# Optimization experiments

Hardware: AMD Instinct MI355X
Metric: run time of the kernel (lower is better)

The kernel has to match this reference:

```python
import math
import jax, jax.numpy as jnp
import numpy as np

TOPK = 2
CAPACITY_FACTOR = 1.25
MIN_CAPACITY = 4


def setup_inputs() -> dict:
    key = jax.random.key(0)
    k1, k2, k3, k4, k5 = jax.random.split(key, 5)
    B, T, H, W, D = 2, 8, 16, 16, 2048
    E, I = 16, 2048
    s = 1.0 / math.sqrt(D)
    return {
        "hidden_states": jax.random.normal(k1, (B, T, H, W, D), dtype=jnp.float32),
        "wg_weight": jax.random.normal(k2, (E, D), dtype=jnp.float32) * s,
        "gate_proj": jax.random.normal(k3, (E, I, D), dtype=jnp.float32) * s,
        "up_proj": jax.random.normal(k4, (E, I, D), dtype=jnp.float32) * s,
        "down_proj": jax.random.normal(k5, (E, D, I), dtype=jnp.float32) * (1.0 / math.sqrt(I)),
    }


def _moe_forward(x, wg, gp, up, dp):
    B, T, H, W, D = x.shape
    S = T * H * W
    # core_shape=(1,1,1): indexing tokens == calculate tokens, flatten (T,H,W)
    tokens = x.reshape(B, S, D).transpose(1, 0, 2).reshape(-1, D)  # (N, D)
    N = tokens.shape[0]
    E = wg.shape[0]

    logits = tokens.astype(jnp.float32) @ wg.T              # (N, E)
    gates = jax.nn.softmax(logits, axis=1)                  # (N, E)

    # static expert capacity: topk * max(ceil(N/E * cf), min_capacity)
    cap = TOPK * max(math.ceil(N / E * CAPACITY_FACTOR), MIN_CAPACITY)

    _, expert_index = jax.lax.top_k(gates, TOPK)            # (N, k)
    expert_mask = jax.nn.one_hot(expert_index, E, dtype=jnp.int32)  # (N, k, E)

    # aux load-balance loss (computed for fidelity)
    mask_aux = expert_mask.max(axis=1).astype(jnp.float32)  # (N, E)
    l_aux = (E ** 2) * jnp.mean(jnp.mean(mask_aux, axis=0) * jnp.mean(gates, axis=0))

    # normalize top-k probabilities (norm_topk_prob=True, topk>1)
    gates_s = jnp.clip(jnp.einsum('nke,ne->n', expert_mask.astype(gates.dtype), gates),
                       jnp.finfo(gates.dtype).eps)
    router_probs = gates / gates_s[:, None]                 # (N, E)

    # token priority: cumsum over (topk*N) flattened in topk-major order
    em = expert_mask.transpose(1, 0, 2).reshape(TOPK * N, E)  # (kN, E)
    tp = jnp.cumsum(em, axis=0) * em - 1
    tp = tp.reshape(TOPK, N, E).transpose(1, 0, 2).max(axis=1)  # (N, E)
    valid = (tp >= 0) & (tp < cap)
    tp = jnp.where(valid, tp, 0)
    dispatch_mask = (tp[:, :, None] == jnp.arange(cap)[None, None, :]) & valid[:, :, None]  # (N,E,C) bool
    combine_weights = router_probs[:, :, None] * dispatch_mask  # (N, E, C)

    # dispatch -> expert FFN (SwiGLU) -> combine
    dm = dispatch_mask.astype(tokens.dtype)
    dispatched = jnp.einsum('nec,nd->ecd', dm, tokens)      # (E, C, D)
    gate_out = jax.nn.silu(jnp.einsum('ecd,eid->eci', dispatched, gp))
    up_out = jnp.einsum('ecd,eid->eci', dispatched, up)
    expert_out = jnp.einsum('eci,edi->ecd', gate_out * up_out, dp)  # (E, C, D)
    combined = jnp.einsum('nec,ecd->nd', combine_weights, expert_out)  # (N, D)

    y = combined.reshape(S, B, D).transpose(1, 0, 2).reshape(B, T, H, W, D)
    return y, l_aux


def reference(hidden_states, wg_weight, gate_proj, up_proj, down_proj):
    y, _l_aux = _moe_forward(hidden_states, wg_weight, gate_proj, up_proj, down_proj)
    return y
```

## Files before the change

kernel.cpp:

```cpp
#include <hip/hip_runtime.h>
#include <hip/hip_bf16.h>
#include <cstdint>
#include <cstddef>

#define NTOK 4096
#define NEXP 16
#define DIM  2048
#define IDIM 2048
#define CAP  640
#define SEQ  2048

typedef float v4f __attribute__((ext_vector_type(4)));
typedef short v8s __attribute__((ext_vector_type(8)));

__device__ __forceinline__ unsigned short f2b(float x) {
    union { float f; unsigned u; } c; c.f = x;
    unsigned r = c.u + 0x7FFFu + ((c.u >> 16) & 1u);
    return (unsigned short)(r >> 16);
}
__device__ __forceinline__ float b2f(unsigned short x) {
    union { unsigned u; float f; } c; c.u = ((unsigned)x) << 16;
    return c.f;
}

__device__ __forceinline__ void async16(const void* g, void* l) {
    __builtin_amdgcn_global_load_lds(
        (const __attribute__((address_space(1))) unsigned int*)g,
        (__attribute__((address_space(3))) unsigned int*)l,
        16, 0, 0);
}

__global__ __launch_bounds__(256) void router_kernel(
    const float* __restrict__ hidden, const float* __restrict__ wg,
    int* __restrict__ top1, int* __restrict__ top2,
    float* __restrict__ w1, float* __restrict__ w2)
{
    int wid  = threadIdx.x >> 6;
    int lane = threadIdx.x & 63;
    int n = blockIdx.x * 4 + wid;
    int e = lane & 15;
    int chunk = lane >> 4;
    const float* tok  = hidden + ((size_t)(n & 1) * SEQ + (n >> 1)) * DIM;
    const float* wrow = wg + (size_t)e * DIM;
    float acc = 0.f;
    int d0 = chunk * (DIM / 4);
    #pragma unroll 4
    for (int d = d0; d < d0 + DIM / 4; d += 4) {
        float4 t4 = *(const float4*)(tok + d);
        float4 g4 = *(const float4*)(wrow + d);
        acc += t4.x * g4.x + t4.y * g4.y + t4.z * g4.z + t4.w * g4.w;
    }
    acc += __shfl_down(acc, 32);
    acc += __shfl_down(acc, 16);
    float v = acc;
    float v1 = v; int i1 = e;
    #pragma unroll
    for (int off = 8; off; off >>= 1) {
        float ov = __shfl_xor(v1, off);
        int   oi = __shfl_xor(i1, off);
        if (ov > v1 || (ov == v1 && oi < i1)) { v1 = ov; i1 = oi; }
    }
    float v2 = (e == i1) ? -INFINITY : v; int i2 = e;
    #pragma unroll
    for (int off = 8; off; off >>= 1) {
        float ov = __shfl_xor(v2, off);
        int   oi = __shfl_xor(i2, off);
        if (ov > v2 || (ov == v2 && oi < i2)) { v2 = ov; i2 = oi; }
    }
    if (lane == 0) {
        float e2v = expf(v2 - v1);
        float inv = 1.f / (1.f + e2v);
        top1[n] = i1; top2[n] = i2;
        w1[n] = inv;  w2[n] = e2v * inv;
    }
}

__global__ __launch_bounds__(1024) void slot_kernel(
    const int* __restrict__ top1, const int* __restrict__ top2,
    int* __restrict__ slot1, int* __restrict__ slot2,
    int* __restrict__ exp_tok, int* __restrict__ counts)
{
    int w = threadIdx.x >> 6;
    int lane = threadIdx.x & 63;
    unsigned long long below = (lane == 0) ? 0ull : ((~0ull) >> (64 - lane));
    int base = 0;
    for (int c = 0; c < NTOK / 64; ++c) {
        int n = c * 64 + lane;
        bool p = (top1[n] == w);
        unsigned long long m = __ballot(p);
        if (p) {
            int s = base + __popcll(m & below);
            slot1[n] = s;
            if (s < CAP) exp_tok[w * CAP + s] = n;
        }
        base += __popcll(m);
    }
    for (int c = 0; c < NTOK / 64; ++c) {
        int n = c * 64 + lane;
        bool p = (top2[n] == w);
        unsigned long long m = __ballot(p);
        if (p) {
            int s = base + __popcll(m & below);
            slot2[n] = s;
            if (s < CAP) exp_tok[w * CAP + s] = n;
        }
        base += __popcll(m);
    }
    if (lane == 0) counts[w] = base < CAP ? base : CAP;
}

__global__ __launch_bounds__(256) void dispatch_kernel(
    const float* __restrict__ hidden, const int* __restrict__ exp_tok,
    const int* __restrict__ counts, unsigned short* __restrict__ disp)
{
    int s = blockIdx.x, e = blockIdx.y;
    unsigned short* dst = disp + ((size_t)e * CAP + s) * DIM + threadIdx.x * 8;
    if (s < counts[e]) {
        int n = exp_tok[e * CAP + s];
        const float* src = hidden + ((size_t)(n & 1) * SEQ + (n >> 1)) * DIM + threadIdx.x * 8;
        float4 a = *(const float4*)src;
        float4 b = *(const float4*)(src + 4);
        v8s o;
        o[0] = (short)f2b(a.x); o[1] = (short)f2b(a.y);
        o[2] = (short)f2b(a.z); o[3] = (short)f2b(a.w);
        o[4] = (short)f2b(b.x); o[5] = (short)f2b(b.y);
        o[6] = (short)f2b(b.z); o[7] = (short)f2b(b.w);
        *(v8s*)dst = o;
    } else {
        v8s z = {0, 0, 0, 0, 0, 0, 0, 0};
        *(v8s*)dst = z;
    }
}

#define BK 64

template<int NW, int ROUNDS>
__device__ __forceinline__ void stage_a(
    const unsigned short* __restrict__ gbase, int grow0, int k0, int rs,
    unsigned short* lds, int wv, int ln)
{
    int sr = ln >> 3;
    int cb = ln & 7;
    #pragma unroll
    for (int p = 0; p < ROUNDS; ++p) {
        int r = p * (NW * 8) + wv * 8 + sr;
        const unsigned short* g = gbase + (size_t)(grow0 + r) * rs + k0 + ((cb ^ (r & 7)) << 3);
        async16(g, lds + (p * (NW * 8) + wv * 8) * 64);
    }
}

template<int NT, int ROUNDS>
__device__ __forceinline__ void issue_bx(
    const float* __restrict__ gbase, int grow0, int k0, int rs,
    float4* regs, int tid)
{
    int cb = tid & 7;
    int r0 = tid >> 3;
    #pragma unroll
    for (int p = 0; p < ROUNDS; ++p) {
        const float* g = gbase + (size_t)(grow0 + p * (NT / 8) + r0) * rs + k0 + (cb << 3);
        regs[2 * p]     = *(const float4*)g;
        regs[2 * p + 1] = *(const float4*)(g + 4);
    }
}

template<int NT, int ROUNDS>
__device__ __forceinline__ void write_bx(
    const float4* regs, unsigned short* lds, int tid)
{
    int cb = tid & 7;
    int r0 = tid >> 3;
    #pragma unroll
    for (int p = 0; p < ROUNDS; ++p) {
        int r = p * (NT / 8) + r0;
        float4 x = regs[2 * p], y = regs[2 * p + 1];
        v8s o;
        o[0] = (short)f2b(x.x); o[1] = (short)f2b(x.y);
        o[2] = (short)f2b(x.z); o[3] = (short)f2b(x.w);
        o[4] = (short)f2b(y.x); o[5] = (short)f2b(y.y);
        o[6] = (short)f2b(y.z); o[7] = (short)f2b(y.w);
        *(v8s*)&lds[r * 64 + ((cb ^ (r & 7)) << 3)] = o;
    }
}

__device__ __forceinline__ void grid_decomp3(int bid, int& mi, int& ni, int& e) {
    int swz = (bid & 7) * 96 + (bid >> 3);
    mi = swz % 3;
    int t = swz / 3;
    ni = t & 15;
    e  = t >> 4;
}

__global__ __launch_bounds__(512, 2) void gateup_kernel(
    const unsigned short* __restrict__ disp, const float* __restrict__ gp,
    const float* __restrict__ up, const int* __restrict__ counts,
    unsigned short* __restrict__ hbuf)
{
    extern __shared__ unsigned short smem[];
    unsigned short* As0 = smem;
    unsigned short* As1 = smem + 16384;
    unsigned short* Bgs = smem + 32768;
    unsigned short* Bus = smem + 40960;
    int mi, ni, e;
    grid_decomp3(blockIdx.x, mi, ni, e);
    int m0 = mi * 256;
    if (m0 >= counts[e]) return;
    int n0 = ni * 128;
    int tid = threadIdx.x;
    int wv = tid >> 6, ln = tid & 63;
    int wm = wv >> 1, wn = wv & 1;
    int lrow = ln & 15, quad = ln >> 4;
    int sw = lrow & 7;

    const unsigned short* Ab = disp + (size_t)e * CAP * DIM;
    const float* Gb = gp + (size_t)e * IDIM * DIM;
    const float* Ub = up + (size_t)e * IDIM * DIM;

    int arow[4], brow[4];
    #pragma unroll
    for (int i = 0; i < 4; ++i) {
        arow[i] = (wm * 64 + i * 16 + lrow) * 64;
        brow[i] = (wn * 64 + i * 16 + lrow) * 64;
    }

    v4f accg[4][4], accu[4][4];
    #pragma unroll
    for (int i = 0; i < 4; ++i)
        #pragma unroll
        for (int j = 0; j < 4; ++j) { accg[i][j] = (v4f)0.f; accu[i][j] = (v4f)0.f; }

    float4 rg[4], ru[4];
    stage_a<8, 4>(Ab, m0, 0, DIM, As0, wv, ln);
    issue_bx<512, 2>(Gb, n0, 0, DIM, rg, tid);
    issue_bx<512, 2>(Ub, n0, 0, DIM, ru, tid);

    for (int k0 = 0; k0 < DIM; k0 += BK) {
        int cur = (k0 >> 6) & 1;
        unsigned short* Ac = cur ? As1 : As0;
        unsigned short* An = cur ? As0 : As1;
        __syncthreads();
        write_bx<512, 2>(rg, Bgs, tid);
        write_bx<512, 2>(ru, Bus, tid);
        __syncthreads();
        int kn = k0 + BK;
        if (kn < DIM) {
            stage_a<8, 4>(Ab, m0, kn, DIM, An, wv, ln);
            issue_bx<512, 2>(Gb, n0, kn, DIM, rg, tid);
            issue_bx<512, 2>(Ub, n0, kn, DIM, ru, tid);
        }
        #pragma unroll
        for (int ks = 0; ks < BK; ks += 32) {
            int cq = ks >> 3;
            v8s a[4];
            #pragma unroll
            for (int i = 0; i < 4; ++i)
                a[i] = *(const v8s*)&Ac[arow[i] + (((cq + quad) ^ sw) << 3)];
            #pragma unroll
            for (int j = 0; j < 4; ++j) {
                v8s bg = *(const v8s*)&Bgs[brow[j] + (((cq + quad) ^ sw) << 3)];
                v8s bu = *(const v8s*)&Bus[brow[j] + (((cq + quad) ^ sw) << 3)];
                #pragma unroll
                for (int i = 0; i < 4; ++i) {
                    accg[i][j] = __builtin_amdgcn_mfma_f32_16x16x32_bf16(a[i], bg, accg[i][j], 0, 0, 0);
                    accu[i][j] = __builtin_amdgcn_mfma_f32_16x16x32_bf16(a[i], bu, accu[i][j], 0, 0, 0);
                }
            }
        }
    }
    unsigned short* hb = hbuf + (size_t)e * CAP * IDIM;
    #pragma unroll
    for (int i = 0; i < 4; ++i)
        #pragma unroll
        for (int j = 0; j < 4; ++j) {
            int row = m0 + wm * 64 + i * 16 + quad * 4;
            int col = n0 + wn * 64 + j * 16 + lrow;
            #pragma unroll
            for (int rg_ = 0; rg_ < 4; ++rg_) {
                if (row + rg_ < CAP) {
                    float g = accg[i][j][rg_], u = accu[i][j][rg_];
                    float hv = (g / (1.f + __expf(-g))) * u;
                    hb[(size_t)(row + rg_) * IDIM + col] = f2b(hv);
                }
            }
        }
}

__global__ __launch_bounds__(256, 2) void down_kernel(
    const unsigned short* __restrict__ hbuf, const float* __restrict__ dp,
    const int* __restrict__ counts, unsigned short* __restrict__ eo)
{
    extern __shared__ unsigned short smem[];
    unsigned short* As0 = smem;
    unsigned short* As1 = smem + 16384;
    unsigned short* Bs  = smem + 32768;
    int mi, ni, e;
    grid_decomp3(blockIdx.x, mi, ni, e);
    int m0 = mi * 256;
    if (m0 >= counts[e]) return;
    int n0 = ni * 128;
    int tid = threadIdx.x;
    int wv = tid >> 6, ln = tid & 63;
    int wm = wv >> 1, wn = wv & 1;
    int lrow = ln & 15, quad = ln >> 4;
    int sw = lrow & 7;

    const unsigned short* Ab = hbuf + (size_t)e * CAP * IDIM;
    const float* Db = dp + (size_t)e * DIM * IDIM;

    int arow[8], brow[4];
    #pragma unroll
    for (int i = 0; i < 8; ++i)
        arow[i] = (wm * 128 + i * 16 + lrow) * 64;
    #pragma unroll
    for (int j = 0; j < 4; ++j)
        brow[j] = (wn * 64 + j * 16 + lrow) * 64;

    v4f acc[8][4];
    #pragma unroll
    for (int i = 0; i < 8; ++i)
        #pragma unroll
        for (int j = 0; j < 4; ++j) acc[i][j] = (v4f)0.f;

    float4 rb[8];
    stage_a<4, 8>(Ab, m0, 0, IDIM, As0, wv, ln);
    issue_bx<256, 4>(Db, n0, 0, IDIM, rb, tid);

    for (int k0 = 0; k0 < IDIM; k0 += BK) {
        int cur = (k0 >> 6) & 1;
        unsigned short* Ac = cur ? As1 : As0;
        unsigned short* An = cur ? As0 : As1;
        __syncthreads();
        write_bx<256, 4>(rb, Bs, tid);
        __syncthreads();
        int kn = k0 + BK;
        if (kn < IDIM) {
            stage_a<4, 8>(Ab, m0, kn, IDIM, An, wv, ln);
            issue_bx<256, 4>(Db, n0, kn, IDIM, rb, tid);
        }
        #pragma unroll
        for (int ks = 0; ks < BK; ks += 32) {
            int cq = ks >> 3;
            v8s a[8];
            #pragma unroll
            for (int i = 0; i < 8; ++i)
                a[i] = *(const v8s*)&Ac[arow[i] + (((cq + quad) ^ sw) << 3)];
            #pragma unroll
            for (int j = 0; j < 4; ++j) {
                v8s b = *(const v8s*)&Bs[brow[j] + (((cq + quad) ^ sw) << 3)];
                #pragma unroll
                for (int i = 0; i < 8; ++i)
                    acc[i][j] = __builtin_amdgcn_mfma_f32_16x16x32_bf16(a[i], b, acc[i][j], 0, 0, 0);
            }
        }
    }
    unsigned short* ob = eo + (size_t)e * CAP * DIM;
    #pragma unroll
    for (int i = 0; i < 8; ++i)
        #pragma unroll
        for (int j = 0; j < 4; ++j) {
            int row = m0 + wm * 128 + i * 16 + quad * 4;
            int col = n0 + wn * 64 + j * 16 + lrow;
            #pragma unroll
            for (int rg_ = 0; rg_ < 4; ++rg_) {
                if (row + rg_ < CAP)
                    ob[(size_t)(row + rg_) * DIM + col] = f2b(acc[i][j][rg_]);
            }
        }
}

__global__ __launch_bounds__(256) void combine_kernel(
    const unsigned short* __restrict__ eo,
    const int* __restrict__ top1, const int* __restrict__ top2,
    const int* __restrict__ slot1, const int* __restrict__ slot2,
    const float* __restrict__ w1, const float* __restrict__ w2,
    float* __restrict__ out)
{
    int n = blockIdx.x;
    int d = threadIdx.x * 8;
    float acc[8];
    #pragma unroll
    for (int i = 0; i < 8; ++i) acc[i] = 0.f;
    int s1 = slot1[n], s2 = slot2[n];
    if (s1 < CAP) {
        const unsigned short* p = eo + ((size_t)top1[n] * CAP + s1) * DIM + d;
        float w = w1[n];
        v8s v = *(const v8s*)p;
        #pragma unroll
        for (int i = 0; i < 8; ++i) acc[i] += w * b2f((unsigned short)v[i]);
    }
    if (s2 < CAP) {
        const unsigned short* p = eo + ((size_t)top2[n] * CAP + s2) * DIM + d;
        float w = w2[n];
        v8s v = *(const v8s*)p;
        #pragma unroll
        for (int i = 0; i < 8; ++i) acc[i] += w * b2f((unsigned short)v[i]);
    }
    float* o = out + ((size_t)(n & 1) * SEQ + (n >> 1)) * DIM + d;
    float4 o0 = {acc[0], acc[1], acc[2], acc[3]};
    float4 o1 = {acc[4], acc[5], acc[6], acc[7]};
    *(float4*)o = o0;
    *(float4*)(o + 4) = o1;
}

extern "C" void kernel_launch(void* const* d_in, const int* in_sizes, int n_in,
                              void* d_out, int out_size, void* d_ws, size_t ws_size,
                              hipStream_t stream) {
    const float* hidden = (const float*)d_in[0];
    const float* wg     = (const float*)d_in[1];
    const float* gp     = (const float*)d_in[2];
    const float* up     = (const float*)d_in[3];
    const float* dp     = (const float*)d_in[4];
    float* out = (float*)d_out;
    char* ws = (char*)d_ws;

    int*   top1    = (int*)(ws + 0);
    int*   top2    = (int*)(ws + 16384);
    float* w1      = (float*)(ws + 32768);
    float* w2      = (float*)(ws + 49152);
    int*   slot1   = (int*)(ws + 65536);
    int*   slot2   = (int*)(ws + 81920);
    int*   counts  = (int*)(ws + 98304);
    int*   exp_tok = (int*)(ws + 98560);
    unsigned short* disp = (unsigned short*)(ws + 262144);
    unsigned short* hbuf = (unsigned short*)(ws + 262144 + 41943040ull);
    unsigned short* eo   = (unsigned short*)(ws + 262144 + 2ull*41943040ull);

    static bool attr_set = false;
    if (!attr_set) {
        hipFuncSetAttribute((const void*)gateup_kernel,
                            hipFuncAttributeMaxDynamicSharedMemorySize, 98304);
        hipFuncSetAttribute((const void*)down_kernel,
                            hipFuncAttributeMaxDynamicSharedMemorySize, 81920);
        attr_set = true;
    }

    const int NB = 3 * 16 * NEXP;

    router_kernel<<<NTOK / 4, 256, 0, stream>>>(hidden, wg, top1, top2, w1, w2);
    slot_kernel<<<1, 1024, 0, stream>>>(top1, top2, slot1, slot2, exp_tok, counts);
    dispatch_kernel<<<dim3(CAP, NEXP), 256, 0, stream>>>(hidden, exp_tok, counts, disp);
    gateup_kernel<<<NB, 512, 98304, stream>>>(disp, gp, up, counts, hbuf);
    down_kernel<<<NB, 256, 81920, stream>>>(hbuf, dp, counts, eo);
    combine_kernel<<<NTOK, 256, 0, stream>>>(eo, top1, top2, slot1, slot2, w1, w2, out);
}
```

Measured before the change: 1.048 ms.

## Triple-buffer down-proj A tiles with 512 threads and packed bf16 conversion

The down-projection kernel moves from 256 to 512 threads, with each wave handling a 64x64 sub-tile instead of 128x64. The A operand becomes a triple-buffered LDS ring and two register sets hold the fp32 weight prefetches, so loads run two K-steps ahead. Custom barriers avoid full memory drains between steps. The float-to-bf16 packing in dispatch and in the weight LDS writes now uses the hardware v_cvt_pk_bf16_f32 instruction, which uses round-to-nearest-even like the old manual routine. The cost is more LDS per block (114688 bytes), which may limit residency to one block per CU despite launch_bounds(512,2).

After: 1.060 ms. No clear change (+1.2%).

```diff
diff --git a/kernel.cpp b/kernel.cpp
--- a/kernel.cpp
+++ b/kernel.cpp
@@ -12,6 +12,7 @@
 
 typedef float v4f __attribute__((ext_vector_type(4)));
 typedef short v8s __attribute__((ext_vector_type(8)));
+typedef unsigned int v4u __attribute__((ext_vector_type(4)));
 
 __device__ __forceinline__ unsigned short f2b(float x) {
     union { float f; unsigned u; } c; c.f = x;
@@ -21,6 +22,11 @@
 __device__ __forceinline__ float b2f(unsigned short x) {
     union { unsigned u; float f; } c; c.u = ((unsigned)x) << 16;
     return c.f;
+}
+__device__ __forceinline__ unsigned cvt2(float a, float b) {
+    unsigned r;
+    asm("v_cvt_pk_bf16_f32 %0, %1, %2" : "=v"(r) : "v"(a), "v"(b));
+    return r;
 }
 
 __device__ __forceinline__ void async16(const void* g, void* l) {
@@ -28,6 +34,19 @@
         (const __attribute__((address_space(1))) unsigned int*)g,
         (__attribute__((address_space(3))) unsigned int*)l,
         16, 0, 0);
+}
+
+__device__ __forceinline__ void barrier_nodrain() {
+    __builtin_amdgcn_sched_barrier(0);
+    __builtin_amdgcn_s_barrier();
+    __builtin_amdgcn_sched_barrier(0);
+}
+__device__ __forceinline__ void lds_publish_barrier() {
+    __builtin_amdgcn_sched_barrier(0);
+    asm volatile("s_waitcnt lgkmcnt(0)");
+    __builtin_amdgcn_sched_barrier(0);
+    __builtin_amdgcn_s_barrier();
+    __builtin_amdgcn_sched_barrier(0);
 }
 
 __global__ __launch_bounds__(256) void router_kernel(
@@ -120,12 +139,10 @@
         const float* src = hidden + ((size_t)(n & 1) * SEQ + (n >> 1)) * DIM + threadIdx.x * 8;
         float4 a = *(const float4*)src;
         float4 b = *(const float4*)(src + 4);
-        v8s o;
-        o[0] = (short)f2b(a.x); o[1] = (short)f2b(a.y);
-        o[2] = (short)f2b(a.z); o[3] = (short)f2b(a.w);
-        o[4] = (short)f2b(b.x); o[5] = (short)f2b(b.y);
-        o[6] = (short)f2b(b.z); o[7] = (short)f2b(b.w);
-        *(v8s*)dst = o;
+        v4u o;
+        o[0] = cvt2(a.x, a.y); o[1] = cvt2(a.z, a.w);
+        o[2] = cvt2(b.x, b.y); o[3] = cvt2(b.z, b.w);
+        *(v4u*)dst = o;
     } else {
         v8s z = {0, 0, 0, 0, 0, 0, 0, 0};
         *(v8s*)dst = z;
@@ -174,12 +191,10 @@
     for (int p = 0; p < ROUNDS; ++p) {
         int r = p * (NT / 8) + r0;
         float4 x = regs[2 * p], y = regs[2 * p + 1];
-        v8s o;
-        o[0] = (short)f2b(x.x); o[1] = (short)f2b(x.y);
-        o[2] = (short)f2b(x.z); o[3] = (short)f2b(x.w);
-        o[4] = (short)f2b(y.x); o[5] = (short)f2b(y.y);
-        o[6] = (short)f2b(y.z); o[7] = (short)f2b(y.w);
-        *(v8s*)&lds[r * 64 + ((cb ^ (r & 7)) << 3)] = o;
+        v4u o;
+        o[0] = cvt2(x.x, x.y); o[1] = cvt2(x.z, x.w);
+        o[2] = cvt2(y.x, y.y); o[3] = cvt2(y.z, y.w);
+        *(v4u*)&lds[r * 64 + ((cb ^ (r & 7)) << 3)] = o;
     }
 }
 
@@ -285,14 +300,32 @@
         }
 }
 
-__global__ __launch_bounds__(256, 2) void down_kernel(
+#define DN_COMPUTE(PA)                                                         \
+    _Pragma("unroll")                                                          \
+    for (int ks = 0; ks < BK; ks += 32) {                                      \
+        int cq = ks >> 3;                                                      \
+        v8s a_[4];                                                             \
+        _Pragma("unroll")                                                      \
+        for (int i = 0; i < 4; ++i)                                            \
+            a_[i] = *(const v8s*)&PA[arow[i] + (((cq + quad) ^ sw) << 3)];     \
+        _Pragma("unroll")                                                      \
+        for (int j = 0; j < 4; ++j) {                                          \
+            v8s b_ = *(const v8s*)&Bs[brow[j] + (((cq + quad) ^ sw) << 3)];    \
+            _Pragma("unroll")                                                  \
+            for (int i = 0; i < 4; ++i)                                        \
+                acc[i][j] = __builtin_amdgcn_mfma_f32_16x16x32_bf16(a_[i], b_, acc[i][j], 0, 0, 0); \
+        }                                                                      \
+    }
+
+__global__ __launch_bounds__(512, 2) void down_kernel(
     const unsigned short* __restrict__ hbuf, const float* __restrict__ dp,
     const int* __restrict__ counts, unsigned short* __restrict__ eo)
 {
     extern __shared__ unsigned short smem[];
-    unsigned short* As0 = smem;
-    unsigned short* As1 = smem + 16384;
-    unsigned short* Bs  = smem + 32768;
+    unsigned short* A0 = smem;
+    unsigned short* A1 = smem + 16384;
+    unsigned short* A2 = smem + 32768;
+    unsigned short* Bs = smem + 49152;
     int mi, ni, e;
     grid_decomp3(blockIdx.x, mi, ni, e);
     int m0 = mi * 256;
@@ -307,58 +340,59 @@
     const unsigned short* Ab = hbuf + (size_t)e * CAP * IDIM;
     const float* Db = dp + (size_t)e * DIM * IDIM;
 
-    int arow[8], brow[4];
-    #pragma unroll
-    for (int i = 0; i < 8; ++i)
-        arow[i] = (wm * 128 + i * 16 + lrow) * 64;
-    #pragma unroll
-    for (int j = 0; j < 4; ++j)
-        brow[j] = (wn * 64 + j * 16 + lrow) * 64;
-
-    v4f acc[8][4];
-    #pragma unroll
-    for (int i = 0; i < 8; ++i)
+    int arow[4], brow[4];
+    #pragma unroll
+    for (int i = 0; i < 4; ++i) {
+        arow[i] = (wm * 64 + i * 16 + lrow) * 64;
+        brow[i] = (wn * 64 + i * 16 + lrow) * 64;
+    }
+
+    v4f acc[4][4];
+    #pragma unroll
+    for (int i = 0; i < 4; ++i)
         #pragma unroll
         for (int j = 0; j < 4; ++j) acc[i][j] = (v4f)0.f;
 
-    float4 rb[8];
-    stage_a<4, 8>(Ab, m0, 0, IDIM, As0, wv, ln);
-    issue_bx<256, 4>(Db, n0, 0, IDIM, rb, tid);
-
-    for (int k0 = 0; k0 < IDIM; k0 += BK) {
-        int cur = (k0 >> 6) & 1;
-        unsigned short* Ac = cur ? As1 : As0;
-        unsigned short* An = cur ? As0 : As1;
-        __syncthreads();
-        write_bx<256, 4>(rb, Bs, tid);
-        __syncthreads();
-        int kn = k0 + BK;
-        if (kn < IDIM) {
-            stage_a<4, 8>(Ab, m0, kn, IDIM, An, wv, ln);
-            issue_bx<256, 4>(Db, n0, kn, IDIM, rb, tid);
-        }
-        #pragma unroll
-        for (int ks = 0; ks < BK; ks += 32) {
-            int cq = ks >> 3;
-            v8s a[8];
-            #pragma unroll
-            for (int i = 0; i < 8; ++i)
-                a[i] = *(const v8s*)&Ac[arow[i] + (((cq + quad) ^ sw) << 3)];
-            #pragma unroll
-            for (int j = 0; j < 4; ++j) {
-                v8s b = *(const v8s*)&Bs[brow[j] + (((cq + quad) ^ sw) << 3)];
-                #pragma unroll
-                for (int i = 0; i < 8; ++i)
-                    acc[i][j] = __builtin_amdgcn_mfma_f32_16x16x32_bf16(a[i], b, acc[i][j], 0, 0, 0);
-            }
-        }
+    float4 rb0[4], rb1[4];
+    stage_a<8, 4>(Ab, m0, 0, IDIM, A0, wv, ln);
+    __builtin_amdgcn_sched_barrier(0);
+    issue_bx<512, 2>(Db, n0, 0, IDIM, rb0, tid);
+    __builtin_amdgcn_sched_barrier(0);
+    stage_a<8, 4>(Ab, m0, BK, IDIM, A1, wv, ln);
+    __builtin_amdgcn_sched_barrier(0);
+    issue_bx<512, 2>(Db, n0, BK, IDIM, rb1, tid);
+
+    unsigned short *pa = A0, *pb = A1, *pc = A2;
+    for (int k0 = 0; k0 < IDIM; k0 += 2 * BK) {
+        barrier_nodrain();
+        write_bx<512, 2>(rb0, Bs, tid);
+        lds_publish_barrier();
+        if (k0 + 2 * BK < IDIM) {
+            stage_a<8, 4>(Ab, m0, k0 + 2 * BK, IDIM, pc, wv, ln);
+            __builtin_amdgcn_sched_barrier(0);
+            issue_bx<512, 2>(Db, n0, k0 + 2 * BK, IDIM, rb0, tid);
+        }
+        __builtin_amdgcn_sched_barrier(0);
+        DN_COMPUTE(pa);
+        { unsigned short* t = pa; pa = pb; pb = pc; pc = t; }
+        barrier_nodrain();
+        write_bx<512, 2>(rb1, Bs, tid);
+        lds_publish_barrier();
+        if (k0 + 3 * BK < IDIM) {
+            stage_a<8, 4>(Ab, m0, k0 + 3 * BK, IDIM, pc, wv, ln);
+            __builtin_amdgcn_sched_barrier(0);
+            issue_bx<512, 2>(Db, n0, k0 + 3 * BK, IDIM, rb1, tid);
+        }
+        __builtin_amdgcn_sched_barrier(0);
+        DN_COMPUTE(pa);
+        { unsigned short* t = pa; pa = pb; pb = pc; pc = t; }
     }
     unsigned short* ob = eo + (size_t)e * CAP * DIM;
     #pragma unroll
-    for (int i = 0; i < 8; ++i)
+    for (int i = 0; i < 4; ++i)
         #pragma unroll
         for (int j = 0; j < 4; ++j) {
-            int row = m0 + wm * 128 + i * 16 + quad * 4;
+            int row = m0 + wm * 64 + i * 16 + quad * 4;
             int col = n0 + wn * 64 + j * 16 + lrow;
             #pragma unroll
             for (int rg_ = 0; rg_ < 4; ++rg_) {
@@ -430,7 +464,7 @@
         hipFuncSetAttribute((const void*)gateup_kernel,
                             hipFuncAttributeMaxDynamicSharedMemorySize, 98304);
         hipFuncSetAttribute((const void*)down_kernel,
-                            hipFuncAttributeMaxDynamicSharedMemorySize, 81920);
+                            hipFuncAttributeMaxDynamicSharedMemorySize, 114688);
         attr_set = true;
     }
 
@@ -440,6 +474,6 @@
     slot_kernel<<<1, 1024, 0, stream>>>(top1, top2, slot1, slot2, exp_tok, counts);
     dispatch_kernel<<<dim3(CAP, NEXP), 256, 0, stream>>>(hidden, exp_tok, counts, disp);
     gateup_kernel<<<NB, 512, 98304, stream>>>(disp, gp, up, counts, hbuf);
-    down_kernel<<<NB, 256, 81920, stream>>>(hbuf, dp, counts, eo);
+    down_kernel<<<NB, 512, 114688, stream>>>(hbuf, dp, counts, eo);
     combine_kernel<<<NTOK, 256, 0, stream>>>(eo, top1, top2, slot1, slot2, w1, w2, out);
 }
```
